# Kernel optimization log

Hardware: AMD Instinct MI355X
Metric: run time of the kernel (lower is better)

The kernel has to match this reference:

```python
import jax, jax.numpy as jnp
import numpy as np

K1, K2, K3 = 6, 4, 3  # knn_graph k (loop=True -> self included, dist 0 is always top)


def _sqdist(a, b):
    # a: [B,N,3], b: [B,M,3] -> [B,N,M] squared euclidean distances
    an = jnp.sum(a * a, -1)[:, :, None]
    bn = jnp.sum(b * b, -1)[:, None, :]
    return an + bn - 2.0 * jnp.einsum('bnd,bmd->bnm', a, b)


def _knn_idx(pos, k):
    # for each point, indices of its k nearest neighbors (self included, loop=True)
    d = _sqdist(pos, pos)                 # [B,N,N]
    _, idx = jax.lax.top_k(-d, k)         # [B,N,k]
    return idx


def _gather(a, idx):
    # a: [B,N,...], idx: [B,...] -> per-cloud gather
    return jax.vmap(lambda ab, ib: ab[ib])(a, idx)


def _fps(pos, m):
    # farthest point sampling on one cloud [N,3], deterministic start at index 0
    min_d = jnp.sum((pos - pos[0]) ** 2, -1)  # [N]

    def step(min_d, _):
        idx = jnp.argmax(min_d)
        d = jnp.sum((pos - pos[idx]) ** 2, -1)
        return jnp.minimum(min_d, d), idx

    _, idxs = jax.lax.scan(step, min_d, None, length=m - 1)
    return jnp.concatenate([jnp.zeros((1,), dtype=idxs.dtype), idxs])


def _pn_layer(h, pos, k, W1, b1, W2, b2):
    # PointNetLayer: gather h_i/h_j/pos_i/pos_j over knn edges, MLP, max-aggregate
    idx = _knn_idx(pos, k)                       # [B,N,k]
    h_j = _gather(h, idx)                        # [B,N,k,C]
    pos_j = _gather(pos, idx)                    # [B,N,k,3]
    rel = pos_j - pos[:, :, None, :]             # pos_j - pos_i
    h_i = jnp.broadcast_to(h[:, :, None, :], h_j.shape)
    inp = jnp.concatenate([h_i, h_j, rel], -1)   # [B,N,k,2C+3]
    msg = jnp.maximum(inp @ W1 + b1, 0.0) @ W2 + b2
    return jnp.max(msg, axis=2)                  # scatter-max == dense max over k


def _forward(x, pos, W11, b11, W12, b12, W21, b21, W22, b22, W31, b31, W32, b32, Wr, br):
    h = jax.nn.relu(_pn_layer(x, pos, K1, W11, b11, W12, b12))
    idx = jax.vmap(lambda p: _fps(p, p.shape[0] // 2))(pos)   # ratio=0.5
    pos, h = _gather(pos, idx), _gather(h, idx)
    h = jax.nn.relu(_pn_layer(h, pos, K2, W21, b21, W22, b22))
    idx = jax.vmap(lambda p: _fps(p, p.shape[0] // 2))(pos)
    pos, h = _gather(pos, idx), _gather(h, idx)
    h = jax.nn.relu(_pn_layer(h, pos, K3, W31, b31, W32, b32))
    g = jnp.max(h, axis=1)                        # global_max_pool
    return g @ Wr + br                            # [B,10]


def _lin(key, fin, fout):
    k1, k2 = jax.random.split(key)
    lim = 1.0 / np.sqrt(fin)
    W = jax.random.uniform(k1, (fin, fout), minval=-lim, maxval=lim, dtype=jnp.float32)
    b = jax.random.uniform(k2, (fout,), minval=-lim, maxval=lim, dtype=jnp.float32)
    return W, b


def setup_inputs() -> dict:
    key = jax.random.key(0)
    ks = jax.random.split(key, 10)
    B, N = 16, 4096
    x = jax.random.normal(ks[0], (B, N, 1), dtype=jnp.float32)
    pos = jax.random.uniform(ks[1], (B, N, 3), dtype=jnp.float32)
    W11, b11 = _lin(ks[2], 1 * 2 + 3, 32)
    W12, b12 = _lin(ks[3], 32, 32)
    W21, b21 = _lin(ks[4], 32 * 2 + 3, 32)
    W22, b22 = _lin(ks[5], 32, 32)
    W31, b31 = _lin(ks[6], 32 * 2 + 3, 32)
    W32, b32 = _lin(ks[7], 32, 32)
    Wr, br = _lin(ks[8], 32, 10)
    return dict(x=x, pos=pos, W11=W11, b11=b11, W12=W12, b12=b12,
                W21=W21, b21=b21, W22=W22, b22=b22,
                W31=W31, b31=b31, W32=W32, b32=b32, Wr=Wr, br=br)


def reference(x, pos, W11, b11, W12, b12, W21, b21, W22, b22, W31, b31, W32, b32, Wr, br):
    return _forward(x, pos, W11, b11, W12, b12, W21, b21, W22, b22,
                    W31, b31, W32, b32, Wr, br)
```

## Files before the change

### kernel.cpp

```cpp
#include <hip/hip_runtime.h>

#define BATCH 16
#define NP1 4096
#define NP2 2048
#define NP3 1024

typedef float v2f __attribute__((ext_vector_type(2)));

__device__ __forceinline__ float f_add(float a, float b) { return __fadd_rn(a, b); }
__device__ __forceinline__ float f_mul(float a, float b) { return __fmul_rn(a, b); }
__device__ __forceinline__ float f_sub(float a, float b) { return __fsub_rn(a, b); }
__device__ __forceinline__ float sqnorm3(float x, float y, float z) {
  return f_add(f_add(f_mul(x, x), f_mul(y, y)), f_mul(z, z));
}

__device__ __forceinline__ unsigned long long u64max(unsigned long long a,
                                                     unsigned long long b) {
  return a > b ? a : b;
}
__device__ __forceinline__ unsigned long long u64min(unsigned long long a,
                                                     unsigned long long b) {
  return a < b ? a : b;
}
__device__ __forceinline__ double dmax(double a, double b) { return __builtin_fmax(a, b); }
__device__ __forceinline__ double dmin(double a, double b) { return __builtin_fmin(a, b); }

template<int CTRL, int RMASK>
__device__ __forceinline__ unsigned long long dpp_u64(unsigned long long k) {
  const int lo = __builtin_amdgcn_update_dpp(0, (int)(unsigned)k, CTRL, RMASK, 0xF, true);
  const int hi = __builtin_amdgcn_update_dpp(0, (int)(unsigned)(k >> 32), CTRL, RMASK, 0xF, true);
  return ((unsigned long long)(unsigned)hi << 32) | (unsigned)lo;
}
template<int CTRL, int RMASK>
__device__ __forceinline__ double dpp_dbl(double v) {
  return __longlong_as_double(
      (long long)dpp_u64<CTRL, RMASK>((unsigned long long)__double_as_longlong(v)));
}


__device__ __forceinline__ void tup_comb(double& a1, double& a2, double b1, double b2) {
  const double hi = dmax(a1, b1);
  const double lo = dmin(a1, b1);
  a2 = dmax(lo, dmax(a2, b2));
  a1 = hi;
}
template<int CTRL, int RMASK>
__device__ __forceinline__ void tup_stage(double& a1, double& a2) {
  const double b1 = dpp_dbl<CTRL, RMASK>(a1);
  const double b2 = dpp_dbl<CTRL, RMASK>(a2);
  tup_comb(a1, a2, b1, b2);
}

template<int N, int M>
__device__ void fps_block(char* __restrict__ smem, const float* __restrict__ P,
                          int* __restrict__ samp, float* __restrict__ pos_out)
{
#pragma clang fp contract(off)
  constexpr int THREADS = 512;
  constexpr int E = N / THREADS;
  constexpr int P2 = E / 2;
  float4* pos4 = (float4*)smem;
  unsigned short* ord = (unsigned short*)(smem + 16 * N);
  int* sampL = (int*)(smem + 18 * N);
  unsigned* cursor = (unsigned*)(smem + 18 * N + 4 * M);
  double* kslots = (double*)(smem + 18 * N + 4 * M + 32);
  float* px = (float*)(smem + 18 * N + 4 * M + 32 + 256);
  float* py = px + N;
  float* pz = py + N;
  const int tid = threadIdx.x;
  const int lane = tid & 63, wv = tid >> 6;
  const int myslot = lane & 7;
  if (tid < 8) cursor[tid] = 0u;
  __syncthreads();
  int oct[E];
#pragma unroll
  for (int e = 0; e < E; ++e) {
    const int t = e * THREADS + tid;
    const float x = P[t * 3], y = P[t * 3 + 1], z = P[t * 3 + 2];
    pos4[t] = make_float4(x, y, z, 0.f);
    px[t] = x; py[t] = y; pz[t] = z;
    oct[e] = (x > 0.5f ? 1 : 0) | (y > 0.5f ? 2 : 0) | (z > 0.5f ? 4 : 0);
    atomicAdd(&cursor[oct[e]], 1u);
  }
  __syncthreads();
  if (tid == 0) {
    unsigned run = 0;
#pragma unroll
    for (int o = 0; o < 8; ++o) { const unsigned c = cursor[o]; cursor[o] = run; run += c; }
  }
  __syncthreads();
#pragma unroll
  for (int e = 0; e < E; ++e) {
    const unsigned d = atomicAdd(&cursor[oct[e]], 1u);
    ord[d] = (unsigned short)(e * THREADS + tid);
  }
  __syncthreads();
  const float4 p0 = pos4[0];
  const float x0 = p0.x, y0 = p0.y, z0 = p0.z;
  v2f X2[P2], Y2[P2], Z2[P2], MD2[P2];
  unsigned ILO[E];
  float mnx = 1e30f, mny = 1e30f, mnz = 1e30f;
  float mxx = -1e30f, mxy = -1e30f, mxz = -1e30f;
  {
    const v2f x0v = {x0, x0}, y0v = {y0, y0}, z0v = {z0, z0};
#pragma unroll
    for (int p = 0; p < P2; ++p) {
      const int q0 = wv * (64 * E) + (2 * p) * 64 + lane;
      const int o0 = ord[q0], o1 = ord[q0 + 64];
      const float4 a0 = pos4[o0], a1 = pos4[o1];
      X2[p] = (v2f){a0.x, a1.x}; Y2[p] = (v2f){a0.y, a1.y}; Z2[p] = (v2f){a0.z, a1.z};
      mnx = fminf(mnx, fminf(a0.x, a1.x)); mxx = fmaxf(mxx, fmaxf(a0.x, a1.x));
      mny = fminf(mny, fminf(a0.y, a1.y)); mxy = fmaxf(mxy, fmaxf(a0.y, a1.y));
      mnz = fminf(mnz, fminf(a0.z, a1.z)); mxz = fmaxf(mxz, fmaxf(a0.z, a1.z));
      const v2f dx = X2[p] - x0v, dy = Y2[p] - y0v, dz = Z2[p] - z0v;
      MD2[p] = (dx * dx + dy * dy) + dz * dz;
      ILO[2 * p]     = 0xFFFFFFFFu - (unsigned)o0;
      ILO[2 * p + 1] = 0xFFFFFFFFu - (unsigned)o1;
    }
  }
#pragma unroll
  for (int off = 1; off < 64; off <<= 1) {
    mnx = fminf(mnx, __shfl_xor(mnx, off)); mxx = fmaxf(mxx, __shfl_xor(mxx, off));
    mny = fminf(mny, __shfl_xor(mny, off)); mxy = fmaxf(mxy, __shfl_xor(mxy, off));
    mnz = fminf(mnz, __shfl_xor(mnz, off)); mxz = fmaxf(mxz, __shfl_xor(mxz, off));
  }
  if (tid == 0) sampL[0] = 0;
  bool dirty = true;
  double W1 = 0.0, W2 = 0.0;
  int s = 1, it = 0;
#pragma unroll 1
  while (s < M) {
    if (dirty) {
      double k[E];
#pragma unroll
      for (int p = 0; p < P2; ++p) {
        k[2 * p] = __longlong_as_double((long long)(
            ((unsigned long long)__float_as_uint(MD2[p].x) << 32) | ILO[2 * p]));
        k[2 * p + 1] = __longlong_as_double((long long)(
            ((unsigned long long)__float_as_uint(MD2[p].y) << 32) | ILO[2 * p + 1]));
      }
      double A1 = dmax(k[0], k[1]), A2 = dmin(k[0], k[1]);
      double B1 = dmax(k[2], k[3]), B2 = dmin(k[2], k[3]);
      double C1 = dmax(k[4], k[5]), C2 = dmin(k[4], k[5]);
      double D1 = dmax(k[6], k[7]), D2 = dmin(k[6], k[7]);
      tup_comb(A1, A2, B1, B2); tup_comb(C1, C2, D1, D2); tup_comb(A1, A2, C1, C2);
      tup_stage<0x111, 0xF>(A1, A2);
      tup_stage<0x112, 0xF>(A1, A2);
      tup_stage<0x114, 0xF>(A1, A2);
      tup_stage<0x118, 0xF>(A1, A2);
      tup_stage<0x142, 0xA>(A1, A2);
      tup_stage<0x143, 0xC>(A1, A2);
      W1 = A1; W2 = A2;
    }
    const int pb = it & 1;
    if (lane == 63) ((double2*)kslots)[pb * 8 + wv] = make_double2(W1, W2);
    __syncthreads();
    double2 tt = ((double2*)kslots)[pb * 8 + myslot];
    const unsigned long long ckey = (unsigned long long)__double_as_longlong(
        (lane & 8) ? tt.y : tt.x);
    const int cidx = (int)(0xFFFFFFFFu - (unsigned)ckey);
    const float cx = px[cidx], cy = py[cidx], cz = pz[cidx];
    double T1 = tt.x, T2 = tt.y;
    tup_stage<0xB1, 0xF>(T1, T2);
    tup_stage<0x4E, 0xF>(T1, T2);
    tup_stage<0x124, 0xF>(T1, T2);
    const unsigned long long g1b = (unsigned long long)__double_as_longlong(T1);
    const unsigned long long g2b = (unsigned long long)__double_as_longlong(T2);
    const int gi1 = (int)(0xFFFFFFFFu - (unsigned)g1b);
    const int gi2 = (int)(0xFFFFFFFFu - (unsigned)g2b);
    const unsigned long long mm1 = __ballot(ckey == g1b);
    const unsigned long long mm2 = __ballot(ckey == g2b);
    const int L1 = (int)__builtin_ctzll(mm1);
    const int L2 = (int)__builtin_ctzll(mm2);
    float4 sp1, sp2;
    sp1.x = __uint_as_float((unsigned)__builtin_amdgcn_readlane((int)__float_as_uint(cx), L1));
    sp1.y = __uint_as_float((unsigned)__builtin_amdgcn_readlane((int)__float_as_uint(cy), L1));
    sp1.z = __uint_as_float((unsigned)__builtin_amdgcn_readlane((int)__float_as_uint(cz), L1));
    sp2.x = __uint_as_float((unsigned)__builtin_amdgcn_readlane((int)__float_as_uint(cx), L2));
    sp2.y = __uint_as_float((unsigned)__builtin_amdgcn_readlane((int)__float_as_uint(cy), L2));
    sp2.z = __uint_as_float((unsigned)__builtin_amdgcn_readlane((int)__float_as_uint(cz), L2));
    const float md2b = __uint_as_float((unsigned)(g2b >> 32));
    const float ddx = f_sub(sp2.x, sp1.x), ddy = f_sub(sp2.y, sp1.y),
                ddz = f_sub(sp2.z, sp1.z);
    const float dchk = f_add(f_add(f_mul(ddx, ddx), f_mul(ddy, ddy)), f_mul(ddz, ddz));
    const bool take2 = (s + 1 < M) && (dchk >= md2b);
    if (tid == 0) { sampL[s] = gi1; if (take2) sampL[s + 1] = gi2; }
    const float wmaxf = __uint_as_float((unsigned)__builtin_amdgcn_readlane(
        (int)(unsigned)((unsigned long long)__double_as_longlong(W1) >> 32), 63));
    const float m1x = fmaxf(fmaxf(f_sub(mnx, sp1.x), f_sub(sp1.x, mxx)), 0.f);
    const float m1y = fmaxf(fmaxf(f_sub(mny, sp1.y), f_sub(sp1.y, mxy)), 0.f);
    const float m1z = fmaxf(fmaxf(f_sub(mnz, sp1.z), f_sub(sp1.z, mxz)), 0.f);
    const bool u1 = sqnorm3(m1x, m1y, m1z) < wmaxf;
    const float m2x = fmaxf(fmaxf(f_sub(mnx, sp2.x), f_sub(sp2.x, mxx)), 0.f);
    const float m2y = fmaxf(fmaxf(f_sub(mny, sp2.y), f_sub(sp2.y, mxy)), 0.f);
    const float m2z = fmaxf(fmaxf(f_sub(mnz, sp2.z), f_sub(sp2.z, mxz)), 0.f);
    const bool u2 = take2 && (sqnorm3(m2x, m2y, m2z) < wmaxf);
    if (u1 | u2) {
      dirty = true;
      if (u1 & u2) {
        const v2f s1x = {sp1.x, sp1.x}, s1y = {sp1.y, sp1.y}, s1z = {sp1.z, sp1.z};
        const v2f s2x = {sp2.x, sp2.x}, s2y = {sp2.y, sp2.y}, s2z = {sp2.z, sp2.z};
#pragma unroll
        for (int p = 0; p < P2; ++p) {
          const v2f dx1 = X2[p] - s1x, dy1 = Y2[p] - s1y, dz1 = Z2[p] - s1z;
          const v2f d1 = (dx1 * dx1 + dy1 * dy1) + dz1 * dz1;
          MD2[p] = __builtin_elementwise_min(MD2[p], d1);
          const v2f dx2 = X2[p] - s2x, dy2 = Y2[p] - s2y, dz2 = Z2[p] - s2z;
          const v2f d2 = (dx2 * dx2 + dy2 * dy2) + dz2 * dz2;
          MD2[p] = __builtin_elementwise_min(MD2[p], d2);
        }
      } else {
        const float4 sp = u1 ? sp1 : sp2;
        const v2f sxv = {sp.x, sp.x}, syv = {sp.y, sp.y}, szv = {sp.z, sp.z};
#pragma unroll
        for (int p = 0; p < P2; ++p) {
          const v2f dx = X2[p] - sxv, dy = Y2[p] - syv, dz = Z2[p] - szv;
          const v2f d = (dx * dx + dy * dy) + dz * dz;
          MD2[p] = __builtin_elementwise_min(MD2[p], d);
        }
      }
    } else {
      dirty = false;
    }
    s += take2 ? 2 : 1;
    ++it;
  }
  __syncthreads();
  for (int s2 = tid; s2 < M; s2 += THREADS) {
    const int g = sampL[s2];
    samp[s2] = g;
    const float4 sp2 = pos4[g];
    pos_out[3 * s2 + 0] = sp2.x;
    pos_out[3 * s2 + 1] = sp2.y;
    pos_out[3 * s2 + 2] = sp2.z;
  }
}

__device__ __forceinline__ float f4c(const float4& v, int c) {
  return c == 0 ? v.x : c == 1 ? v.y : c == 2 ? v.z : v.w;
}
__device__ __forceinline__ void fma4(float4& a, float v, const float4& w) {
  a.x += v * w.x; a.y += v * w.y; a.z += v * w.z; a.w += v * w.w;
}

template<int K, int C>
__device__ void pn_compute(
    const float4* __restrict__ sW1, const float4* __restrict__ sW2,
    const float* __restrict__ sb1, const float* __restrict__ sb2,
    const float* __restrict__ P, const float* __restrict__ Hsrc,
    const int* __restrict__ hmap, int i, float xi, float yi, float zi,
    const int* kn, float* __restrict__ outrow)
{
  float4 abase[8];
#pragma unroll
  for (int o = 0; o < 8; ++o)
    abase[o] = make_float4(sb1[4 * o], sb1[4 * o + 1], sb1[4 * o + 2], sb1[4 * o + 3]);
  if constexpr (C == 1) {
    const float v = Hsrc[hmap ? hmap[i] : i];
#pragma unroll
    for (int o = 0; o < 8; ++o) fma4(abase[o], v, sW1[o]);
  } else {
    const int ri = hmap ? hmap[i] : i;
    const float4* Hi = (const float4*)(Hsrc + (size_t)ri * C);
#pragma unroll
    for (int c4 = 0; c4 < C / 4; ++c4) {
      const float4 hv = Hi[c4];
#pragma unroll
      for (int q = 0; q < 4; ++q) {
        const float v = f4c(hv, q);
#pragma unroll
        for (int o = 0; o < 8; ++o) fma4(abase[o], v, sW1[(4 * c4 + q) * 8 + o]);
      }
    }
  }
  float4 best[8];
#pragma unroll
  for (int o = 0; o < 8; ++o)
    best[o] = make_float4(-__builtin_inff(), -__builtin_inff(), -__builtin_inff(), -__builtin_inff());

  auto edge_pair = [&](int j0, int j1) {
    float4 a0[8], a1[8];
#pragma unroll
    for (int o = 0; o < 8; ++o) { a0[o] = abase[o]; a1[o] = abase[o]; }
    const float rx0 = P[j0 * 3] - xi, ry0 = P[j0 * 3 + 1] - yi, rz0 = P[j0 * 3 + 2] - zi;
    const float rx1 = P[j1 * 3] - xi, ry1 = P[j1 * 3 + 1] - yi, rz1 = P[j1 * 3 + 2] - zi;
    if constexpr (C == 1) {
      const float v0 = Hsrc[hmap ? hmap[j0] : j0], v1 = Hsrc[hmap ? hmap[j1] : j1];
#pragma unroll
      for (int o = 0; o < 8; ++o) {
        const float4 w = sW1[C * 8 + o];
        fma4(a0[o], v0, w); fma4(a1[o], v1, w);
      }
    } else {
      const int r0i = hmap ? hmap[j0] : j0, r1i = hmap ? hmap[j1] : j1;
      const float4* Hj0 = (const float4*)(Hsrc + (size_t)r0i * C);
      const float4* Hj1 = (const float4*)(Hsrc + (size_t)r1i * C);
#pragma unroll
      for (int c4 = 0; c4 < C / 4; ++c4) {
        const float4 h0 = Hj0[c4], h1 = Hj1[c4];
#pragma unroll
        for (int q = 0; q < 4; ++q) {
          const float v0 = f4c(h0, q), v1 = f4c(h1, q);
#pragma unroll
          for (int o = 0; o < 8; ++o) {
            const float4 w = sW1[(C + 4 * c4 + q) * 8 + o];
            fma4(a0[o], v0, w); fma4(a1[o], v1, w);
          }
        }
      }
    }
    const float r0[3] = {rx0, ry0, rz0}, r1[3] = {rx1, ry1, rz1};
#pragma unroll
    for (int r = 0; r < 3; ++r) {
#pragma unroll
      for (int o = 0; o < 8; ++o) {
        const float4 w = sW1[(2 * C + r) * 8 + o];
        fma4(a0[o], r0[r], w); fma4(a1[o], r1[r], w);
      }
    }
#pragma unroll
    for (int o = 0; o < 8; ++o) {
      a0[o].x = fmaxf(a0[o].x, 0.f); a0[o].y = fmaxf(a0[o].y, 0.f);
      a0[o].z = fmaxf(a0[o].z, 0.f); a0[o].w = fmaxf(a0[o].w, 0.f);
      a1[o].x = fmaxf(a1[o].x, 0.f); a1[o].y = fmaxf(a1[o].y, 0.f);
      a1[o].z = fmaxf(a1[o].z, 0.f); a1[o].w = fmaxf(a1[o].w, 0.f);
    }
#pragma unroll
    for (int hf = 0; hf < 2; ++hf) {
      float4 m0[4], m1[4];
#pragma unroll
      for (int o4 = 0; o4 < 4; ++o4) {
        const int c0 = 16 * hf + 4 * o4;
        m0[o4] = make_float4(sb2[c0], sb2[c0 + 1], sb2[c0 + 2], sb2[c0 + 3]);
        m1[o4] = m0[o4];
      }
#pragma unroll
      for (int c = 0; c < 32; ++c) {
        const float v0 = f4c(a0[c >> 2], c & 3), v1 = f4c(a1[c >> 2], c & 3);
#pragma unroll
        for (int o4 = 0; o4 < 4; ++o4) {
          const float4 w = sW2[c * 8 + hf * 4 + o4];
          fma4(m0[o4], v0, w); fma4(m1[o4], v1, w);
        }
      }
#pragma unroll
      for (int o4 = 0; o4 < 4; ++o4) {
        float4& bb = best[hf * 4 + o4];
        bb.x = fmaxf(bb.x, fmaxf(m0[o4].x, m1[o4].x));
        bb.y = fmaxf(bb.y, fmaxf(m0[o4].y, m1[o4].y));
        bb.z = fmaxf(bb.z, fmaxf(m0[o4].z, m1[o4].z));
        bb.w = fmaxf(bb.w, fmaxf(m0[o4].w, m1[o4].w));
      }
    }
  };

#pragma unroll
  for (int e = 0; e + 1 < K; e += 2) edge_pair(kn[e], kn[e + 1]);

  float4* ho = (float4*)outrow;
#pragma unroll
  for (int o = 0; o < 8; ++o)
    ho[o] = make_float4(fmaxf(best[o].x, 0.0f), fmaxf(best[o].y, 0.0f),
                        fmaxf(best[o].z, 0.0f), fmaxf(best[o].w, 0.0f));
}

template<int K, int NC, int C, int THREADS>
__device__ void fused_knn_pn(char* __restrict__ smem,
    const float* __restrict__ P, const float* __restrict__ Hsrc,
    const int* __restrict__ hmap,
    const float* __restrict__ W1, const float* __restrict__ b1,
    const float* __restrict__ W2, const float* __restrict__ b2,
    float* __restrict__ hout, int s)
{
  constexpr int CIN = 2 * C + 3;
  float4* tile = (float4*)smem;
  float4* sW1 = (float4*)(smem + 16 * 1024);
  float4* sW2 = sW1 + CIN * 8;
  float* sb1 = (float*)(sW2 + 32 * 8);
  float* sb2 = sb1 + 32;
  const int tid = threadIdx.x;
  for (int t = tid; t < CIN * 8; t += THREADS) sW1[t] = ((const float4*)W1)[t];
  for (int t = tid; t < 32 * 8; t += THREADS) sW2[t] = ((const float4*)W2)[t];
  if (tid < 32) { sb1[tid] = b1[tid]; sb2[tid] = b2[tid]; }

  const float xi = P[s * 3], yi = P[s * 3 + 1], zi = P[s * 3 + 2];
  const float ni = sqnorm3(xi, yi, zi);
  float bd[K]; int bj[K];
#pragma unroll
  for (int t = 0; t < K; ++t) { bd[t] = __builtin_inff(); bj[t] = 0; }
  for (int base = 0; base < NC; base += 1024) {
    __syncthreads();
    for (int t = tid; t < 1024; t += THREADS) {
      const float* q = P + (size_t)(base + t) * 3;
      const float x = q[0], y = q[1], z = q[2];
      tile[t] = make_float4(x, y, z, sqnorm3(x, y, z));
    }
    __syncthreads();
#pragma unroll 1
    for (int t = 0; t < 1024; t += 8) {
      float dv[8];
#pragma unroll
      for (int u = 0; u < 8; ++u) {
        const float4 q = tile[t + u];
        const float dot = f_add(f_add(f_mul(xi, q.x), f_mul(yi, q.y)), f_mul(zi, q.z));
        dv[u] = f_sub(f_add(ni, q.w), f_mul(2.0f, dot));
      }
#pragma unroll
      for (int u = 0; u < 8; ++u) {
        if (dv[u] < bd[K - 1]) {
          bd[K - 1] = dv[u]; bj[K - 1] = base + t + u;
#pragma unroll
          for (int r = K - 1; r > 0; --r) {
            if (bd[r] < bd[r - 1]) {
              float td = bd[r]; bd[r] = bd[r - 1]; bd[r - 1] = td;
              int   tj = bj[r]; bj[r] = bj[r - 1]; bj[r - 1] = tj;
            } else break;
          }
        }
      }
    }
  }
  pn_compute<K, C>(sW1, sW2, sb1, sb2, P, Hsrc, hmap, s, xi, yi, zi, bj,
                   hout + (size_t)s * 32);
}

template<int K, int NC>
__device__ void fused_knn_pn_quad(char* __restrict__ smem,
    const float* __restrict__ P, const float* __restrict__ Hsrc,
    const int* __restrict__ hmap,
    const float* __restrict__ W1, const float* __restrict__ b1,
    const float* __restrict__ W2, const float* __restrict__ b2,
    float* __restrict__ hout, int s, int q)
{
  constexpr int THREADS = 256;
  constexpr int RQ = NC / 4;
  constexpr int CIN = 67;
  float4* tile = (float4*)smem;
  float4* sW1 = (float4*)(smem + 16 * (NC + 4));
  float4* sW2 = sW1 + CIN * 8;
  float* sb1 = (float*)(sW2 + 32 * 8);
  float* sb2 = sb1 + 32;
  const int tid = threadIdx.x;

  for (int t = tid; t < NC; t += THREADS) {
    const float* c = P + (size_t)t * 3;
    const float x = c[0], y = c[1], z = c[2];
    tile[t + t / RQ] = make_float4(x, y, z, sqnorm3(x, y, z));
  }
  for (int t = tid; t < CIN * 8; t += THREADS) sW1[t] = ((const float4*)W1)[t];
  for (int t = tid; t < 32 * 8; t += THREADS) sW2[t] = ((const float4*)W2)[t];
  if (tid < 32) { sb1[tid] = b1[tid]; sb2[tid] = b2[tid]; }
  __syncthreads();

  const float4 qv = tile[s + s / RQ];
  const float xi = qv.x, yi = qv.y, zi = qv.z, ni = qv.w;

  const int ri = hmap ? hmap[s] : s;
  float4 hi4[8];
  {
    const float4* Hi = (const float4*)(Hsrc + (size_t)ri * 32);
#pragma unroll
    for (int c4 = 0; c4 < 8; ++c4) hi4[c4] = Hi[c4];
  }

  float bd[4]; int bj[4];
#pragma unroll
  for (int t = 0; t < 4; ++t) { bd[t] = __builtin_inff(); bj[t] = 0; }
  const int sbase = q * (RQ + 1);
#pragma unroll 1
  for (int t = 0; t < RQ; t += 8) {
    float dv[8];
#pragma unroll
    for (int u = 0; u < 8; ++u) {
      const float4 c = tile[sbase + t + u];
      const float dot = f_add(f_add(f_mul(xi, c.x), f_mul(yi, c.y)), f_mul(zi, c.z));
      dv[u] = f_sub(f_add(ni, c.w), f_mul(2.0f, dot));
    }
#pragma unroll
    for (int u = 0; u < 8; ++u) {
      if (dv[u] < bd[3]) {
        bd[3] = dv[u]; bj[3] = q * RQ + t + u;
#pragma unroll
        for (int r = 3; r > 0; --r) {
          if (bd[r] < bd[r - 1]) {
            float td = bd[r]; bd[r] = bd[r - 1]; bd[r - 1] = td;
            int   tj = bj[r]; bj[r] = bj[r - 1]; bj[r - 1] = tj;
          } else break;
        }
      }
    }
  }
  unsigned long long a0, a1, a2, a3;
  {
    auto mk = [](float d, int j) {
      unsigned u = __float_as_uint(d);
      u ^= (unsigned)((int)u >> 31) | 0x80000000u;
      return ((unsigned long long)u << 32) | (unsigned)j;
    };
    a0 = mk(bd[0], bj[0]); a1 = mk(bd[1], bj[1]);
    a2 = mk(bd[2], bj[2]); a3 = mk(bd[3], bj[3]);
  }
  {
    const unsigned long long b0 = __shfl_xor(a0, 1), b1_ = __shfl_xor(a1, 1),
                             b2_ = __shfl_xor(a2, 1), b3_ = __shfl_xor(a3, 1);
    const unsigned long long t0 = u64min(a0, b3_), t1 = u64min(a1, b2_),
                             t2 = u64min(a2, b1_), t3 = u64min(a3, b0);
    const unsigned long long u0 = u64min(t0, t2), u2 = u64max(t0, t2),
                             u1 = u64min(t1, t3), u3 = u64max(t1, t3);
    a0 = u64min(u0, u1); a1 = u64max(u0, u1);
    a2 = u64min(u2, u3); a3 = u64max(u2, u3);
  }
  {
    const unsigned long long b0 = __shfl_xor(a0, 2), b1_ = __shfl_xor(a1, 2),
                             b2_ = __shfl_xor(a2, 2), b3_ = __shfl_xor(a3, 2);
    const unsigned long long t0 = u64min(a0, b3_), t1 = u64min(a1, b2_),
                             t2 = u64min(a2, b1_), t3 = u64min(a3, b0);
    const unsigned long long u0 = u64min(t0, t2), u2 = u64max(t0, t2),
                             u1 = u64min(t1, t3), u3 = u64max(t1, t3);
    a0 = u64min(u0, u1); a1 = u64max(u0, u1);
    a2 = u64min(u2, u3); a3 = u64max(u2, u3);
  }
  const int e = (q < K) ? q : (K - 1);
  const unsigned long long ke = (e == 0) ? a0 : (e == 1) ? a1 : (e == 2) ? a2 : a3;
  const int jn = (int)(unsigned)ke;

  const int rj = hmap ? hmap[jn] : jn;
  float4 hj4[8];
  {
    const float4* Hj = (const float4*)(Hsrc + (size_t)rj * 32);
#pragma unroll
    for (int c4 = 0; c4 < 8; ++c4) hj4[c4] = Hj[c4];
  }
  float4 acc[8];
#pragma unroll
  for (int o = 0; o < 8; ++o)
    acc[o] = make_float4(sb1[4 * o], sb1[4 * o + 1], sb1[4 * o + 2], sb1[4 * o + 3]);
#pragma unroll
  for (int c4 = 0; c4 < 8; ++c4) {
    const float4 hv = hi4[c4];
#pragma unroll
    for (int t = 0; t < 4; ++t) {
      const float v = f4c(hv, t);
#pragma unroll
      for (int o = 0; o < 8; ++o) fma4(acc[o], v, sW1[(4 * c4 + t) * 8 + o]);
    }
  }
#pragma unroll
  for (int c4 = 0; c4 < 8; ++c4) {
    const float4 hv = hj4[c4];
#pragma unroll
    for (int t = 0; t < 4; ++t) {
      const float v = f4c(hv, t);
#pragma unroll
      for (int o = 0; o < 8; ++o) fma4(acc[o], v, sW1[(32 + 4 * c4 + t) * 8 + o]);
    }
  }
  const float4 cj = tile[jn + jn / RQ];
  const float r3[3] = {cj.x - xi, cj.y - yi, cj.z - zi};
#pragma unroll
  for (int r = 0; r < 3; ++r)
#pragma unroll
    for (int o = 0; o < 8; ++o) fma4(acc[o], r3[r], sW1[(64 + r) * 8 + o]);
#pragma unroll
  for (int o = 0; o < 8; ++o) {
    acc[o].x = fmaxf(acc[o].x, 0.f); acc[o].y = fmaxf(acc[o].y, 0.f);
    acc[o].z = fmaxf(acc[o].z, 0.f); acc[o].w = fmaxf(acc[o].w, 0.f);
  }
  float4 m[8];
#pragma unroll
  for (int o = 0; o < 8; ++o)
    m[o] = make_float4(sb2[4 * o], sb2[4 * o + 1], sb2[4 * o + 2], sb2[4 * o + 3]);
#pragma unroll
  for (int c = 0; c < 32; ++c) {
    const float v = f4c(acc[c >> 2], c & 3);
#pragma unroll
    for (int o = 0; o < 8; ++o) fma4(m[o], v, sW2[c * 8 + o]);
  }
#pragma unroll
  for (int o = 0; o < 8; ++o) {
    float4 v = m[o];
    v.x = fmaxf(v.x, __shfl_xor(v.x, 1)); v.y = fmaxf(v.y, __shfl_xor(v.y, 1));
    v.z = fmaxf(v.z, __shfl_xor(v.z, 1)); v.w = fmaxf(v.w, __shfl_xor(v.w, 1));
    v.x = fmaxf(v.x, __shfl_xor(v.x, 2)); v.y = fmaxf(v.y, __shfl_xor(v.y, 2));
    v.z = fmaxf(v.z, __shfl_xor(v.z, 2)); v.w = fmaxf(v.w, __shfl_xor(v.w, 2));
    m[o] = v;
  }
  float4* ho = (float4*)(hout + (size_t)s * 32);
  {
    const float4 v0 = m[2 * q], v1 = m[2 * q + 1];
    ho[2 * q] = make_float4(fmaxf(v0.x, 0.f), fmaxf(v0.y, 0.f),
                            fmaxf(v0.z, 0.f), fmaxf(v0.w, 0.f));
    ho[2 * q + 1] = make_float4(fmaxf(v1.x, 0.f), fmaxf(v1.y, 0.f),
                                fmaxf(v1.z, 0.f), fmaxf(v1.w, 0.f));
  }
}

__global__ __launch_bounds__(512) void megaA(
    const float* __restrict__ x, const float* __restrict__ pos,
    const float* __restrict__ W11, const float* __restrict__ b11,
    const float* __restrict__ W12, const float* __restrict__ b12,
    int* __restrict__ samp1, float* __restrict__ pos2, float* __restrict__ h1full)
{
  __shared__ __align__(16) char smem[131392];
  if (blockIdx.x < BATCH) {
    const int b = blockIdx.x;
    fps_block<NP1, NP2>(smem, pos + (size_t)b * NP1 * 3, samp1 + b * NP2,
                        pos2 + (size_t)b * NP2 * 3);
  } else {
    const int id = blockIdx.x - BATCH;
    const int b = id >> 3;
    const int s = (id & 7) * 512 + threadIdx.x;
    fused_knn_pn<6, NP1, 1, 512>(smem, pos + (size_t)b * NP1 * 3, x + (size_t)b * NP1,
                                 nullptr, W11, b11, W12, b12,
                                 h1full + (size_t)b * NP1 * 32, s);
  }
}

__global__ __launch_bounds__(256) void megaB(
    const float* __restrict__ pos2, const int* __restrict__ samp1,
    const float* __restrict__ h1full,
    const float* __restrict__ W21, const float* __restrict__ b21,
    const float* __restrict__ W22, const float* __restrict__ b22,
    float* __restrict__ h2out)
{
  __shared__ __align__(16) char smem[(2048 + 4) * 16 + 67 * 8 * 16 + 32 * 8 * 16 + 256];
  const int b = blockIdx.x >> 4;
  const int s = ((blockIdx.x & 15) << 6) + (threadIdx.x >> 2);
  const int q = threadIdx.x & 3;
  fused_knn_pn_quad<4, NP2>(smem, pos2 + (size_t)b * NP2 * 3,
                            h1full + (size_t)b * NP1 * 32, samp1 + b * NP2,
                            W21, b21, W22, b22, h2out + (size_t)b * NP3 * 32, s, q);
}

__global__ __launch_bounds__(256) void megaC(
    const float* __restrict__ pos2, const float* __restrict__ h2out,
    const float* __restrict__ W31, const float* __restrict__ b31,
    const float* __restrict__ W32, const float* __restrict__ b32,
    float* __restrict__ h3full)
{
  __shared__ __align__(16) char smem[(1024 + 4) * 16 + 67 * 8 * 16 + 32 * 8 * 16 + 256];
  const int b = blockIdx.x >> 4;
  const int s = ((blockIdx.x & 15) << 6) + (threadIdx.x >> 2);
  const int q = threadIdx.x & 3;
  fused_knn_pn_quad<3, NP3>(smem, pos2 + (size_t)b * NP2 * 3,
                            h2out + (size_t)b * NP3 * 32, nullptr,
                            W31, b31, W32, b32, h3full + (size_t)b * NP3 * 32, s, q);
}

__global__ __launch_bounds__(256) void final_kernel(
    const float* __restrict__ h, const float* __restrict__ Wr,
    const float* __restrict__ br, float* __restrict__ out)
{
  __shared__ float red[8][32];
  __shared__ float g[32];
  const int b = blockIdx.x;
  const int c = threadIdx.x & 31, grp = threadIdx.x >> 5;
  const float* H = h + (size_t)b * NP3 * 32;
  float m = -__builtin_inff();
  for (int r = grp; r < NP3; r += 8) m = fmaxf(m, H[r * 32 + c]);
  red[grp][c] = m;
  __syncthreads();
  if (threadIdx.x < 32) {
    float v = red[0][c];
#pragma unroll
    for (int w = 1; w < 8; ++w) v = fmaxf(v, red[w][c]);
    g[c] = v;
  }
  __syncthreads();
  if (threadIdx.x < 10) {
    float v = br[threadIdx.x];
#pragma unroll
    for (int cc = 0; cc < 32; ++cc) v += g[cc] * Wr[cc * 10 + threadIdx.x];
    out[b * 10 + threadIdx.x] = v;
  }
}

extern "C" void kernel_launch(void* const* d_in, const int* in_sizes, int n_in,
                              void* d_out, int out_size, void* d_ws, size_t ws_size,
                              hipStream_t stream) {
  const float* x   = (const float*)d_in[0];
  const float* pos = (const float*)d_in[1];
  const float* W11 = (const float*)d_in[2];
  const float* b11 = (const float*)d_in[3];
  const float* W12 = (const float*)d_in[4];
  const float* b12 = (const float*)d_in[5];
  const float* W21 = (const float*)d_in[6];
  const float* b21 = (const float*)d_in[7];
  const float* W22 = (const float*)d_in[8];
  const float* b22 = (const float*)d_in[9];
  const float* W31 = (const float*)d_in[10];
  const float* b31 = (const float*)d_in[11];
  const float* W32 = (const float*)d_in[12];
  const float* b32 = (const float*)d_in[13];
  const float* Wr  = (const float*)d_in[14];
  const float* br  = (const float*)d_in[15];
  float* out = (float*)d_out;

  char* p = (char*)d_ws;
  auto alloc = [&](size_t bytes) {
    char* r = p; p += (bytes + 255) & ~(size_t)255; return r;
  };
  int*   samp1  = (int*)  alloc(sizeof(int)   * BATCH * NP2);
  float* pos2   = (float*)alloc(sizeof(float) * BATCH * NP2 * 3);
  float* h1full = (float*)alloc(sizeof(float) * BATCH * NP1 * 32);
  float* h2out  = (float*)alloc(sizeof(float) * BATCH * NP3 * 32);
  float* h3full = (float*)alloc(sizeof(float) * BATCH * NP3 * 32);

  megaA<<<BATCH + BATCH * (NP1 / 512), 512, 0, stream>>>(
      x, pos, W11, b11, W12, b12, samp1, pos2, h1full);
  megaB<<<BATCH * 16, 256, 0, stream>>>(
      pos2, samp1, h1full, W21, b21, W22, b22, h2out);
  megaC<<<BATCH * 16, 256, 0, stream>>>(
      pos2, h2out, W31, b31, W32, b32, h3full);
  final_kernel<<<BATCH, 256, 0, stream>>>(h3full, Wr, br, out);
}
```

Baseline: 1.377 ms.

## Publish FPS winner coordinates with per-wave slot records instead of SoA lookup

In the FPS loop, each wave now finds the coordinates of its top-2 candidates in registers, using a wave-uniform index match. It writes them into a per-wave shared-memory slot record next to the keys. After the barrier, lanes read the candidate coordinates directly from these records instead of doing a dependent indexed load from separate px/py/pz arrays, and the first cross-slot reduction stage uses an LDS read in place of a DPP stage. This removes the SoA coordinate copies, shrinking megaA's shared memory, and shortens the serial per-iteration latency chain. The cost is an extra unrolled compare/select loop per wave each iteration.

```diff
diff --git a/kernel.cpp b/kernel.cpp
--- a/kernel.cpp
+++ b/kernel.cpp
@@ -50,6 +50,8 @@
   const double b2 = dpp_dbl<CTRL, RMASK>(a2);
   tup_comb(a1, a2, b1, b2);
 }
+
+struct __align__(16) SlotRec { double2 k; float4 p1, p2; };
 
 template<int N, int M>
 __device__ void fps_block(char* __restrict__ smem, const float* __restrict__ P,
@@ -63,10 +65,7 @@
   unsigned short* ord = (unsigned short*)(smem + 16 * N);
   int* sampL = (int*)(smem + 18 * N);
   unsigned* cursor = (unsigned*)(smem + 18 * N + 4 * M);
-  double* kslots = (double*)(smem + 18 * N + 4 * M + 32);
-  float* px = (float*)(smem + 18 * N + 4 * M + 32 + 256);
-  float* py = px + N;
-  float* pz = py + N;
+  SlotRec* slots = (SlotRec*)(smem + 18 * N + 4 * M + 32);
   const int tid = threadIdx.x;
   const int lane = tid & 63, wv = tid >> 6;
   const int myslot = lane & 7;
@@ -78,7 +77,6 @@
     const int t = e * THREADS + tid;
     const float x = P[t * 3], y = P[t * 3 + 1], z = P[t * 3 + 2];
     pos4[t] = make_float4(x, y, z, 0.f);
-    px[t] = x; py[t] = y; pz[t] = z;
     oct[e] = (x > 0.5f ? 1 : 0) | (y > 0.5f ? 2 : 0) | (z > 0.5f ? 4 : 0);
     atomicAdd(&cursor[oct[e]], 1u);
   }
@@ -152,22 +150,49 @@
       tup_stage<0x143, 0xC>(A1, A2);
       W1 = A1; W2 = A2;
     }
+    const unsigned long long w1b = (unsigned long long)__double_as_longlong(W1);
+    const unsigned long long w2b = (unsigned long long)__double_as_longlong(W2);
+    const unsigned w1lo = (unsigned)__builtin_amdgcn_readlane((int)(unsigned)w1b, 63);
+    const unsigned w1hi = (unsigned)__builtin_amdgcn_readlane((int)(unsigned)(w1b >> 32), 63);
+    const unsigned w2lo = (unsigned)__builtin_amdgcn_readlane((int)(unsigned)w2b, 63);
     const int pb = it & 1;
-    if (lane == 63) ((double2*)kslots)[pb * 8 + wv] = make_double2(W1, W2);
+    SlotRec* mySlot = &slots[pb * 8 + wv];
+    if (lane == 63) mySlot->k = make_double2(W1, W2);
+    {
+      bool has1 = false, has2 = false;
+      float a1x = 0, a1y = 0, a1z = 0, a2x = 0, a2y = 0, a2z = 0;
+#pragma unroll
+      for (int e = 0; e < E; ++e) {
+        if (ILO[e] == w1lo) {
+          has1 = true;
+          a1x = X2[e >> 1][e & 1]; a1y = Y2[e >> 1][e & 1]; a1z = Z2[e >> 1][e & 1];
+        }
+        if (ILO[e] == w2lo) {
+          has2 = true;
+          a2x = X2[e >> 1][e & 1]; a2y = Y2[e >> 1][e & 1]; a2z = Z2[e >> 1][e & 1];
+        }
+      }
+      if (has1) mySlot->p1 = make_float4(a1x, a1y, a1z, 0.f);
+      if (has2) mySlot->p2 = make_float4(a2x, a2y, a2z, 0.f);
+    }
     __syncthreads();
-    double2 tt = ((double2*)kslots)[pb * 8 + myslot];
-    const unsigned long long ckey = (unsigned long long)__double_as_longlong(
-        (lane & 8) ? tt.y : tt.x);
-    const int cidx = (int)(0xFFFFFFFFu - (unsigned)ckey);
-    const float cx = px[cidx], cy = py[cidx], cz = pz[cidx];
-    double T1 = tt.x, T2 = tt.y;
-    tup_stage<0xB1, 0xF>(T1, T2);
+    const double2 sk = slots[pb * 8 + myslot].k;
+    const double2 nk = slots[pb * 8 + (myslot ^ 1)].k;
+    const float4 q1 = slots[pb * 8 + myslot].p1;
+    const float4 q2 = slots[pb * 8 + myslot].p2;
+    double T1 = sk.x, T2 = sk.y;
+    tup_comb(T1, T2, nk.x, nk.y);
     tup_stage<0x4E, 0xF>(T1, T2);
     tup_stage<0x124, 0xF>(T1, T2);
     const unsigned long long g1b = (unsigned long long)__double_as_longlong(T1);
     const unsigned long long g2b = (unsigned long long)__double_as_longlong(T2);
     const int gi1 = (int)(0xFFFFFFFFu - (unsigned)g1b);
     const int gi2 = (int)(0xFFFFFFFFu - (unsigned)g2b);
+    const bool hi8 = (lane & 8) != 0;
+    const unsigned long long ckey = (unsigned long long)__double_as_longlong(hi8 ? sk.y : sk.x);
+    const float cx = hi8 ? q2.x : q1.x;
+    const float cy = hi8 ? q2.y : q1.y;
+    const float cz = hi8 ? q2.z : q1.z;
     const unsigned long long mm1 = __ballot(ckey == g1b);
     const unsigned long long mm2 = __ballot(ckey == g2b);
     const int L1 = (int)__builtin_ctzll(mm1);
@@ -185,8 +210,7 @@
     const float dchk = f_add(f_add(f_mul(ddx, ddx), f_mul(ddy, ddy)), f_mul(ddz, ddz));
     const bool take2 = (s + 1 < M) && (dchk >= md2b);
     if (tid == 0) { sampL[s] = gi1; if (take2) sampL[s + 1] = gi2; }
-    const float wmaxf = __uint_as_float((unsigned)__builtin_amdgcn_readlane(
-        (int)(unsigned)((unsigned long long)__double_as_longlong(W1) >> 32), 63));
+    const float wmaxf = __uint_as_float(w1hi);
     const float m1x = fmaxf(fmaxf(f_sub(mnx, sp1.x), f_sub(sp1.x, mxx)), 0.f);
     const float m1y = fmaxf(fmaxf(f_sub(mny, sp1.y), f_sub(sp1.y, mxy)), 0.f);
     const float m1z = fmaxf(fmaxf(f_sub(mnz, sp1.z), f_sub(sp1.z, mxz)), 0.f);
@@ -601,7 +625,7 @@
     const float* __restrict__ W12, const float* __restrict__ b12,
     int* __restrict__ samp1, float* __restrict__ pos2, float* __restrict__ h1full)
 {
-  __shared__ __align__(16) char smem[131392];
+  __shared__ __align__(16) char smem[82752];
   if (blockIdx.x < BATCH) {
     const int b = blockIdx.x;
     fps_block<NP1, NP2>(smem, pos + (size_t)b * NP1 * 3, samp1 + b * NP2,
```

Result: slower. 1.713 ms (+24.4%).
